# Performance work log

Measured on AMD Instinct MI355X. Metric: run time of the kernel, lower is better.

The kernel has to match this reference:

```python
import jax, jax.numpy as jnp
import numpy as np

N = 50000          # nodes
E = 500000         # edges (before self-loops)
G = 64             # graphs in batch
SC = 96            # scalar features
D = 32             # embedding dim
IN_DIM = SC + 5 * D  # 256
C = 128            # hidden_channels
H1 = 4             # heads in conv1
NUM_CLASSES = 5
V_OP, V_SRC, V_SINK, V_STR, V_PAY = 256, 512, 512, 128, 1024


def setup_inputs() -> dict:
    key = jax.random.key(0)
    ks = jax.random.split(key, 32)
    inp = {}
    inp['x_scalar'] = jax.random.normal(ks[0], (N, SC), jnp.float32)
    inp['x_opcode'] = jax.random.randint(ks[1], (N, 16), 0, V_OP)
    inp['x_source'] = jax.random.randint(ks[2], (N, 8), 0, V_SRC)
    inp['x_sink'] = jax.random.randint(ks[3], (N, 8), 0, V_SINK)
    inp['x_string_manip'] = jax.random.randint(ks[4], (N, 8), 0, V_STR)
    inp['x_payload'] = jax.random.randint(ks[5], (N, 8), 0, V_PAY)
    inp['edge_index'] = jax.random.randint(ks[6], (2, E), 0, N)
    # sorted graph ids with every graph non-empty
    inp['batch'] = (jnp.arange(N) * G) // N
    # learned params
    s = 0.05
    inp['emb_opcode'] = jax.random.normal(ks[7], (V_OP, D), jnp.float32)
    inp['emb_source'] = jax.random.normal(ks[8], (V_SRC, D), jnp.float32)
    inp['emb_sink'] = jax.random.normal(ks[9], (V_SINK, D), jnp.float32)
    inp['emb_string'] = jax.random.normal(ks[10], (V_STR, D), jnp.float32)
    inp['emb_payload'] = jax.random.normal(ks[11], (V_PAY, D), jnp.float32)
    inp['ln_g'] = jnp.ones((IN_DIM,), jnp.float32)
    inp['ln_b'] = jnp.zeros((IN_DIM,), jnp.float32)
    inp['W1'] = jax.random.normal(ks[12], (IN_DIM, H1 * C), jnp.float32) * s
    inp['att_src1'] = jax.random.normal(ks[13], (H1, C), jnp.float32) * s
    inp['att_dst1'] = jax.random.normal(ks[14], (H1, C), jnp.float32) * s
    inp['b1'] = jnp.zeros((H1 * C,), jnp.float32)
    inp['W2'] = jax.random.normal(ks[15], (H1 * C, C), jnp.float32) * s
    inp['att_src2'] = jax.random.normal(ks[16], (1, C), jnp.float32) * s
    inp['att_dst2'] = jax.random.normal(ks[17], (1, C), jnp.float32) * s
    inp['b2'] = jnp.zeros((C,), jnp.float32)
    inp['Wc1'] = jax.random.normal(ks[18], (C, C // 2), jnp.float32) * s
    inp['bc1'] = jnp.zeros((C // 2,), jnp.float32)
    inp['Wc2'] = jax.random.normal(ks[19], (C // 2, NUM_CLASSES), jnp.float32) * s
    inp['bc2'] = jnp.zeros((NUM_CLASSES,), jnp.float32)
    return inp


def _emb_feat(table, idx):
    # masked mean over the list dim; index 0 is padding
    e = table[idx]                                  # [N, L, D]
    mask = (idx != 0)[..., None].astype(e.dtype)    # [N, L, 1]
    return (e * mask).sum(1) / (mask.sum(1) + 1e-9)


def _layernorm(x, g, b, eps=1e-5):
    mu = x.mean(-1, keepdims=True)
    var = ((x - mu) ** 2).mean(-1, keepdims=True)
    return (x - mu) * jax.lax.rsqrt(var + eps) * g + b


def _gat_conv(x, W, att_src, att_dst, bias, src, dst, heads, out_ch, concat):
    n = x.shape[0]
    h = (x @ W).reshape(n, heads, out_ch)              # [N,H,C]
    a_src = (h * att_src).sum(-1)                      # [N,H]
    a_dst = (h * att_dst).sum(-1)                      # [N,H]
    e = jax.nn.leaky_relu(a_src[src] + a_dst[dst], 0.2)  # [E,H]
    m = jax.ops.segment_max(e, dst, num_segments=n)
    e = jnp.exp(e - m[dst])
    denom = jax.ops.segment_sum(e, dst, num_segments=n)
    alpha = e / (denom[dst] + 1e-16)                   # segment softmax over in-edges
    msg = h[src] * alpha[:, :, None]                   # [E,H,C]
    out = jax.ops.segment_sum(msg, dst, num_segments=n)  # [N,H,C]
    out = out.reshape(n, heads * out_ch) if concat else out.mean(1)
    return out + bias


def reference(x_scalar, x_opcode, x_source, x_sink, x_string_manip, x_payload,
              edge_index, batch,
              emb_opcode, emb_source, emb_sink, emb_string, emb_payload,
              ln_g, ln_b, W1, att_src1, att_dst1, b1,
              W2, att_src2, att_dst2, b2, Wc1, bc1, Wc2, bc2):
    n = x_scalar.shape[0]
    feats = jnp.concatenate([
        x_scalar,
        _emb_feat(emb_opcode, x_opcode),
        _emb_feat(emb_source, x_source),
        _emb_feat(emb_sink, x_sink),
        _emb_feat(emb_string, x_string_manip),
        _emb_feat(emb_payload, x_payload),
    ], axis=1)
    feats = _layernorm(feats, ln_g, ln_b)
    # add self loops (PyG GATConv default)
    loop = jnp.arange(n)
    src = jnp.concatenate([edge_index[0], loop])
    dst = jnp.concatenate([edge_index[1], loop])
    x = jax.nn.elu(_gat_conv(feats, W1, att_src1, att_dst1, b1, src, dst, H1, C, True))
    x = jax.nn.elu(_gat_conv(x, W2, att_src2, att_dst2, b2, src, dst, 1, C, True))
    # global max pool per graph (dropout layers are identity at inference)
    xp = jax.ops.segment_max(x, batch, num_segments=G)  # [G,C]
    hcls = jax.nn.relu(xp @ Wc1 + bc1)
    return hcls @ Wc2 + bc2
```

## Files before the change

### kernel.cpp

```cpp
#include <hip/hip_runtime.h>
#include <hip/hip_bf16.h>
#include <float.h>


#define LEAKY(e) ((e) > 0.f ? (e) : 0.2f * (e))
#define POOL_CH 32

typedef _Float16 half8 __attribute__((ext_vector_type(8)));
typedef float floatx4 __attribute__((ext_vector_type(4)));

__device__ __forceinline__ void async_copy16(const _Float16* gsrc,
                                             const _Float16* ldst) {
  __builtin_amdgcn_global_load_lds(
      (const __attribute__((address_space(1))) unsigned int*)gsrc,
      (__attribute__((address_space(3))) unsigned int*)ldst, 16, 0, 0);
}

__global__ __launch_bounds__(256) void feats_kernel(
    const float* __restrict__ xs, const int* __restrict__ xo,
    const int* __restrict__ xsrc, const int* __restrict__ xsk,
    const int* __restrict__ xst, const int* __restrict__ xp,
    const float* __restrict__ eo, const float* __restrict__ es,
    const float* __restrict__ ek, const float* __restrict__ et,
    const float* __restrict__ ep, const float* __restrict__ lng,
    const float* __restrict__ lnb, _Float16* __restrict__ feats, int n) {
  int node = blockIdx.x * 4 + (threadIdx.x >> 6);
  if (node >= n) return;
  int l = threadIdx.x & 63;

  int myidx = 0;
  if (l < 16)      myidx = xo[node * 16 + l];
  else if (l < 24) myidx = xsrc[node * 8 + (l - 16)];
  else if (l < 32) myidx = xsk[node * 8 + (l - 24)];
  else if (l < 40) myidx = xst[node * 8 + (l - 32)];
  else if (l < 48) myidx = xp[node * 8 + (l - 40)];

  const float* xrow = xs + (size_t)node * 96;
  float v0 = xrow[l];
  float v1, v2, v3;

  bool hi = (l >= 32);
  int d = l & 31;

  {
    float s = 0.f, c = 0.f;
#pragma unroll
    for (int j = 0; j < 16; j++) {
      int id = __shfl(myidx, j);
      if (hi && id != 0) { s += eo[(size_t)id * 32 + d]; c += 1.f; }
    }
    float sc = hi ? 0.f : xrow[64 + l];
    v1 = hi ? (s / (c + 1e-9f)) : sc;
  }
  {
    const float* tab = hi ? ek : es;
    int base = hi ? 24 : 16;
    float s = 0.f, c = 0.f;
#pragma unroll
    for (int j = 0; j < 8; j++) {
      int id = __shfl(myidx, base + j);
      if (id != 0) { s += tab[(size_t)id * 32 + d]; c += 1.f; }
    }
    v2 = s / (c + 1e-9f);
  }
  {
    const float* tab = hi ? ep : et;
    int base = hi ? 40 : 32;
    float s = 0.f, c = 0.f;
#pragma unroll
    for (int j = 0; j < 8; j++) {
      int id = __shfl(myidx, base + j);
      if (id != 0) { s += tab[(size_t)id * 32 + d]; c += 1.f; }
    }
    v3 = s / (c + 1e-9f);
  }

  float sum = v0 + v1 + v2 + v3;
  for (int o = 32; o; o >>= 1) sum += __shfl_xor(sum, o);
  float mu = sum * (1.f / 256.f);

  float d0 = v0 - mu, d1 = v1 - mu, d2 = v2 - mu, d3 = v3 - mu;
  float q = d0 * d0 + d1 * d1 + d2 * d2 + d3 * d3;
  for (int o = 32; o; o >>= 1) q += __shfl_xor(q, o);
  float rstd = rsqrtf(q * (1.f / 256.f) + 1e-5f);

  _Float16* frow = feats + (size_t)node * 256;
  frow[l]       = (_Float16)(d0 * rstd * lng[l] + lnb[l]);
  frow[64 + l]  = (_Float16)(d1 * rstd * lng[64 + l] + lnb[64 + l]);
  frow[128 + l] = (_Float16)(d2 * rstd * lng[128 + l] + lnb[128 + l]);
  frow[192 + l] = (_Float16)(d3 * rstd * lng[192 + l] + lnb[192 + l]);
}

__global__ __launch_bounds__(256) void transpose_both_f16(
    const float* __restrict__ W1, _Float16* __restrict__ Wt1,
    const float* __restrict__ W2, _Float16* __restrict__ Wt2) {
  int t = blockIdx.x * 256 + threadIdx.x;
  if (t < 256 * 512) {
    int n = t / 256, k = t - n * 256;
    Wt1[t] = (_Float16)W1[(size_t)k * 512 + n];
  } else {
    int u = t - 256 * 512;
    int n = u / 512, k = u - n * 512;
    Wt2[u] = (_Float16)W2[(size_t)k * 128 + n];
  }
}

__global__ __launch_bounds__(256) void gemm_f16_att(
    const _Float16* __restrict__ A, const _Float16* __restrict__ Bt,
    _Float16* __restrict__ C, const float* __restrict__ att_src,
    const float* __restrict__ att_dst, float* __restrict__ a_src_out,
    float* __restrict__ a_dst_out, int astride, int K, int N) {
  __shared__ __attribute__((aligned(16))) _Float16 As[128 * 32];
  __shared__ __attribute__((aligned(16))) _Float16 Bs[128 * 32];
  int m0 = blockIdx.y * 128;
  int n0 = blockIdx.x * 128;
  int tid = threadIdx.x;
  int wave = tid >> 6, lane = tid & 63;
  int wm = (wave >> 1) * 64, wn = (wave & 1) * 64;
  int lr = lane & 15, lq = lane >> 4;
  int wbase = tid & ~63;

  floatx4 acc[4][4] = {};

  for (int k0 = 0; k0 < K; k0 += 32) {
#pragma unroll
    for (int c = 0; c < 2; c++) {
      int sid = c * 256 + tid;
      int row = sid >> 2;
      int cs = (sid & 3) ^ (row & 3);
      const _Float16* ga = A + (size_t)(m0 + row) * K + k0 + cs * 8;
      const _Float16* gb = Bt + (size_t)(n0 + row) * K + k0 + cs * 8;
      async_copy16(ga, As + (size_t)(c * 256 + wbase) * 8);
      async_copy16(gb, Bs + (size_t)(c * 256 + wbase) * 8);
    }
    __syncthreads();

    half8 af[4], bf[4];
#pragma unroll
    for (int i = 0; i < 4; i++) {
      int row = wm + i * 16 + lr;
      af[i] = *(const half8*)(As + ((row << 2) + (lq ^ (row & 3))) * 8);
    }
#pragma unroll
    for (int j = 0; j < 4; j++) {
      int row = wn + j * 16 + lr;
      bf[j] = *(const half8*)(Bs + ((row << 2) + (lq ^ (row & 3))) * 8);
    }
#pragma unroll
    for (int i = 0; i < 4; i++)
#pragma unroll
      for (int j = 0; j < 4; j++)
        acc[i][j] =
            __builtin_amdgcn_mfma_f32_16x16x32_f16(af[i], bf[j], acc[i][j], 0, 0, 0);
    __syncthreads();
  }

#pragma unroll
  for (int i = 0; i < 4; i++) {
    int rbase = m0 + wm + i * 16 + lq * 4;
#pragma unroll
    for (int r = 0; r < 4; r++) {
      int row = rbase + r;
#pragma unroll
      for (int j = 0; j < 4; j++) {
        int col = n0 + wn + j * 16 + lr;
        C[(size_t)row * N + col] = (_Float16)acc[i][j][r];
      }
    }
  }

  float asv[4], adv[4];
#pragma unroll
  for (int j = 0; j < 4; j++) {
    int col = n0 + wn + j * 16 + lr;
    asv[j] = att_src[col];
    adv[j] = att_dst[col];
  }
  float ps[4][4], pd[4][4];
#pragma unroll
  for (int i = 0; i < 4; i++)
#pragma unroll
    for (int r = 0; r < 4; r++) {
      float s = 0.f, d = 0.f;
#pragma unroll
      for (int j = 0; j < 4; j++) {
        s += acc[i][j][r] * asv[j];
        d += acc[i][j][r] * adv[j];
      }
#pragma unroll
      for (int o = 1; o < 16; o <<= 1) {
        s += __shfl_xor(s, o);
        d += __shfl_xor(d, o);
      }
      ps[i][r] = s;
      pd[i][r] = d;
    }
  float* sred = (float*)&As[0];
  if (wn == 64 && lr == 0) {
#pragma unroll
    for (int i = 0; i < 4; i++)
#pragma unroll
      for (int r = 0; r < 4; r++) {
        int rl = wm + i * 16 + lq * 4 + r;
        sred[rl * 2] = ps[i][r];
        sred[rl * 2 + 1] = pd[i][r];
      }
  }
  __syncthreads();
  if (wn == 0 && lr == 0) {
    int hsel = n0 >> 7;
#pragma unroll
    for (int i = 0; i < 4; i++)
#pragma unroll
      for (int r = 0; r < 4; r++) {
        int rl = wm + i * 16 + lq * 4 + r;
        int row = m0 + rl;
        a_src_out[(size_t)row * astride + hsel] = ps[i][r] + sred[rl * 2];
        a_dst_out[(size_t)row * astride + hsel] = pd[i][r] + sred[rl * 2 + 1];
      }
  }
}

__global__ __launch_bounds__(256) void hist_kernel(const int* __restrict__ dst,
                                                   int* __restrict__ deg, int E) {
  int t = blockIdx.x * 256 + threadIdx.x;
  if (t < E) atomicAdd(&deg[dst[t]], 1);
}

__global__ __launch_bounds__(256) void scan_a(const int* __restrict__ deg,
                                              int* __restrict__ rowptr,
                                              int* __restrict__ bsum, int n) {
  __shared__ int sh[256];
  int b = blockIdx.x, t = threadIdx.x;
  int i = b * 256 + t;
  int v = (i < n) ? deg[i] + 1 : 0;
  sh[t] = v;
  __syncthreads();
  int x = v;
  for (int o = 1; o < 256; o <<= 1) {
    int y = (t >= o) ? sh[t - o] : 0;
    __syncthreads();
    x += y;
    sh[t] = x;
    __syncthreads();
  }
  if (i < n) rowptr[i] = x - v;
  if (t == 255) bsum[b] = x;
}

__global__ __launch_bounds__(256) void scan_b(int* __restrict__ bsum, int nb) {
  __shared__ int sh[256];
  int t = threadIdx.x;
  int v = (t < nb) ? bsum[t] : 0;
  sh[t] = v;
  __syncthreads();
  int x = v;
  for (int o = 1; o < 256; o <<= 1) {
    int y = (t >= o) ? sh[t - o] : 0;
    __syncthreads();
    x += y;
    sh[t] = x;
    __syncthreads();
  }
  if (t < nb) bsum[t] = x - v;
}

__global__ __launch_bounds__(256) void scan_c(int* __restrict__ rowptr,
                                              const int* __restrict__ bsum,
                                              int n, int total) {
  int i = blockIdx.x * 256 + threadIdx.x;
  if (i < n) rowptr[i] += bsum[blockIdx.x];
  else if (i == n) rowptr[n] = total;
}

__global__ __launch_bounds__(256) void fill_kernel(
    const int* __restrict__ src, const int* __restrict__ dst,
    const int* __restrict__ rowptr, int* __restrict__ cnt,
    int* __restrict__ csr_src, int E, int n) {
  int t = blockIdx.x * 256 + threadIdx.x;
  if (t < E) {
    int d = dst[t];
    int pos = rowptr[d] + atomicAdd(&cnt[d], 1);
    csr_src[pos] = src[t];
  } else if (t < E + n) {
    int i = t - E;
    csr_src[rowptr[i + 1] - 1] = i;
  }
}

__global__ __launch_bounds__(256) void gat1_agg(
    const _Float16* __restrict__ h1, const float* __restrict__ asrc,
    const float* __restrict__ adst, const int* __restrict__ rowptr,
    const int* __restrict__ csr_src, const float* __restrict__ bias,
    _Float16* __restrict__ out, int n) {
  int node = blockIdx.x * 4 + (threadIdx.x >> 6);
  if (node >= n) return;
  int l = threadIdx.x & 63;
  int hh = l >> 4;
  int li = l & 15;
  int r0 = rowptr[node];
  int deg = rowptr[node + 1] - r0;
  int cb = l * 8;

  float acc[8] = {};

  if (deg <= 64) {
    float adm = adst[node * 4 + hh];
    int s_reg[4];
    float ww[4];
    float m = -1e30f;
#pragma unroll
    for (int c = 0; c < 4; c++) {
      int k = c * 16 + li;
      int s = (k < deg) ? csr_src[r0 + k] : -1;
      s_reg[c] = s;
      float e = -1e30f;
      if (s >= 0) {
        float t = asrc[(size_t)s * 4 + hh] + adm;
        e = LEAKY(t);
      }
      ww[c] = e;
      m = fmaxf(m, e);
    }
#pragma unroll
    for (int o = 1; o < 16; o <<= 1) m = fmaxf(m, __shfl_xor(m, o));
    float sum = 0.f;
#pragma unroll
    for (int c = 0; c < 4; c++) {
      float w = (s_reg[c] >= 0) ? __expf(ww[c] - m) : 0.f;
      ww[c] = w;
      sum += w;
    }
#pragma unroll
    for (int o = 1; o < 16; o <<= 1) sum += __shfl_xor(sum, o);
    float sinv = 1.f / (sum + 1e-16f);
#pragma unroll
    for (int c = 0; c < 4; c++) ww[c] *= sinv;

#pragma unroll
    for (int c = 0; c < 4; c++) {
      int base = c * 16;
      if (base >= deg) break;
      int lim = min(16, deg - base);
      int jl = 0;
      for (; jl + 4 <= lim; jl += 4) {
        int s0 = __shfl(s_reg[c], jl);
        int s1 = __shfl(s_reg[c], jl + 1);
        int s2 = __shfl(s_reg[c], jl + 2);
        int s3 = __shfl(s_reg[c], jl + 3);
        float w0 = __shfl(ww[c], hh * 16 + jl);
        float w1 = __shfl(ww[c], hh * 16 + jl + 1);
        float w2 = __shfl(ww[c], hh * 16 + jl + 2);
        float w3 = __shfl(ww[c], hh * 16 + jl + 3);
        const half8 hv0 = *(const half8*)(h1 + (size_t)s0 * 512 + cb);
        const half8 hv1 = *(const half8*)(h1 + (size_t)s1 * 512 + cb);
        const half8 hv2 = *(const half8*)(h1 + (size_t)s2 * 512 + cb);
        const half8 hv3 = *(const half8*)(h1 + (size_t)s3 * 512 + cb);
#pragma unroll
        for (int q = 0; q < 8; q++)
          acc[q] += w0 * (float)hv0[q] + w1 * (float)hv1[q] +
                    w2 * (float)hv2[q] + w3 * (float)hv3[q];
      }
      for (; jl < lim; jl++) {
        int s0 = __shfl(s_reg[c], jl);
        float w0 = __shfl(ww[c], hh * 16 + jl);
        const half8 hv0 = *(const half8*)(h1 + (size_t)s0 * 512 + cb);
#pragma unroll
        for (int q = 0; q < 8; q++) acc[q] += w0 * (float)hv0[q];
      }
    }
  } else {
    float4 ad4 = *(const float4*)(adst + node * 4);
    float adv[4] = {ad4.x, ad4.y, ad4.z, ad4.w};
    float m[4] = {-1e30f, -1e30f, -1e30f, -1e30f};
    for (int k = l; k < deg; k += 64) {
      int s = csr_src[r0 + k];
      float4 av = *(const float4*)(asrc + (size_t)s * 4);
      float e;
      e = LEAKY(av.x + adv[0]); m[0] = fmaxf(m[0], e);
      e = LEAKY(av.y + adv[1]); m[1] = fmaxf(m[1], e);
      e = LEAKY(av.z + adv[2]); m[2] = fmaxf(m[2], e);
      e = LEAKY(av.w + adv[3]); m[3] = fmaxf(m[3], e);
    }
    for (int o = 1; o < 64; o <<= 1) {
#pragma unroll
      for (int h = 0; h < 4; h++) m[h] = fmaxf(m[h], __shfl_xor(m[h], o));
    }
    float sum[4] = {0.f, 0.f, 0.f, 0.f};
    for (int k = l; k < deg; k += 64) {
      int s = csr_src[r0 + k];
      float4 av = *(const float4*)(asrc + (size_t)s * 4);
      float e;
      e = LEAKY(av.x + adv[0]); sum[0] += __expf(e - m[0]);
      e = LEAKY(av.y + adv[1]); sum[1] += __expf(e - m[1]);
      e = LEAKY(av.z + adv[2]); sum[2] += __expf(e - m[2]);
      e = LEAKY(av.w + adv[3]); sum[3] += __expf(e - m[3]);
    }
    for (int o = 1; o < 64; o <<= 1) {
#pragma unroll
      for (int h = 0; h < 4; h++) sum[h] += __shfl_xor(sum[h], o);
    }
    float mm = m[hh];
    float sinv = 1.f / (sum[hh] + 1e-16f);
    float adm = adv[hh];
    for (int k = 0; k < deg; k++) {
      int s = csr_src[r0 + k];
      float a = asrc[(size_t)s * 4 + hh];
      float e = LEAKY(a + adm);
      float w = __expf(e - mm) * sinv;
      const half8 hv = *(const half8*)(h1 + (size_t)s * 512 + cb);
#pragma unroll
      for (int q = 0; q < 8; q++) acc[q] += w * (float)hv[q];
    }
  }

  const float* bp = bias + cb;
  half8 ov;
#pragma unroll
  for (int j = 0; j < 8; j++) {
    float r = acc[j] + bp[j];
    ov[j] = (_Float16)(r > 0.f ? r : (__expf(r) - 1.f));
  }
  *(half8*)(out + (size_t)node * 512 + cb) = ov;
}

__global__ __launch_bounds__(256) void gat2_agg(
    const _Float16* __restrict__ h2, const float* __restrict__ asrc,
    const float* __restrict__ adst, const int* __restrict__ rowptr,
    const int* __restrict__ csr_src, const float* __restrict__ bias,
    float* __restrict__ out, int n) {
  int node = blockIdx.x * 4 + (threadIdx.x >> 6);
  if (node >= n) return;
  int l = threadIdx.x & 63;
  int r0 = rowptr[node];
  int deg = rowptr[node + 1] - r0;
  int cb = l * 2;
  float a0 = 0.f, a1 = 0.f;

  if (deg <= 64) {
    float ad = adst[node];
    int s = (l < deg) ? csr_src[r0 + l] : -1;
    float e = -1e30f;
    if (s >= 0) {
      float t = asrc[s] + ad;
      e = LEAKY(t);
    }
    float m = e;
    for (int o = 1; o < 64; o <<= 1) m = fmaxf(m, __shfl_xor(m, o));
    float w = (s >= 0) ? __expf(e - m) : 0.f;
    float sum = w;
    for (int o = 1; o < 64; o <<= 1) sum += __shfl_xor(sum, o);
    w *= 1.f / (sum + 1e-16f);
    int j = 0;
    for (; j + 4 <= deg; j += 4) {
      int s0 = __shfl(s, j);
      int s1 = __shfl(s, j + 1);
      int s2 = __shfl(s, j + 2);
      int s3 = __shfl(s, j + 3);
      float w0 = __shfl(w, j);
      float w1 = __shfl(w, j + 1);
      float w2 = __shfl(w, j + 2);
      float w3 = __shfl(w, j + 3);
      const _Float16* hp0 = h2 + (size_t)s0 * 128 + cb;
      const _Float16* hp1 = h2 + (size_t)s1 * 128 + cb;
      const _Float16* hp2 = h2 + (size_t)s2 * 128 + cb;
      const _Float16* hp3 = h2 + (size_t)s3 * 128 + cb;
      float p00 = (float)hp0[0], p01 = (float)hp0[1];
      float p10 = (float)hp1[0], p11 = (float)hp1[1];
      float p20 = (float)hp2[0], p21 = (float)hp2[1];
      float p30 = (float)hp3[0], p31 = (float)hp3[1];
      a0 += w0 * p00 + w1 * p10 + w2 * p20 + w3 * p30;
      a1 += w0 * p01 + w1 * p11 + w2 * p21 + w3 * p31;
    }
    for (; j < deg; j++) {
      int sj = __shfl(s, j);
      float wj = __shfl(w, j);
      const _Float16* hp = h2 + (size_t)sj * 128 + cb;
      a0 += wj * (float)hp[0];
      a1 += wj * (float)hp[1];
    }
  } else {
    float ad = adst[node];
    float m = -1e30f;
    for (int k = l; k < deg; k += 64) {
      int s = csr_src[r0 + k];
      float e = LEAKY(asrc[s] + ad);
      m = fmaxf(m, e);
    }
    for (int o = 1; o < 64; o <<= 1) m = fmaxf(m, __shfl_xor(m, o));
    float sum = 0.f;
    for (int k = l; k < deg; k += 64) {
      int s = csr_src[r0 + k];
      float e = LEAKY(asrc[s] + ad);
      sum += __expf(e - m);
    }
    for (int o = 1; o < 64; o <<= 1) sum += __shfl_xor(sum, o);
    float sinv = 1.f / (sum + 1e-16f);
    for (int k = 0; k < deg; k++) {
      int s = csr_src[r0 + k];
      float e = LEAKY(asrc[s] + ad);
      float w = __expf(e - m) * sinv;
      const _Float16* hp = h2 + (size_t)s * 128 + cb;
      a0 += w * (float)hp[0];
      a1 += w * (float)hp[1];
    }
  }

  float ra = a0 + bias[cb];
  float rb = a1 + bias[cb + 1];
  out[(size_t)node * 128 + cb]     = ra > 0.f ? ra : (__expf(ra) - 1.f);
  out[(size_t)node * 128 + cb + 1] = rb > 0.f ? rb : (__expf(rb) - 1.f);
}

__device__ inline int lower_bound_i(const int* a, int n, int v) {
  int lo = 0, hi = n;
  while (lo < hi) {
    int mid = (lo + hi) >> 1;
    if (a[mid] < v) lo = mid + 1; else hi = mid;
  }
  return lo;
}

__global__ __launch_bounds__(128) void pool_partial(
    const float* __restrict__ x2, const int* __restrict__ batch,
    float* __restrict__ partial, int n) {
  int g = blockIdx.y;
  int j = blockIdx.x;
  int t = threadIdx.x;
  int start = lower_bound_i(batch, n, g);
  int end = lower_bound_i(batch, n, g + 1);
  int len = end - start;
  int c0 = start + (int)((long long)len * j / POOL_CH);
  int c1 = start + (int)((long long)len * (j + 1) / POOL_CH);
  float m = -FLT_MAX;
  for (int i = c0; i < c1; i++) m = fmaxf(m, x2[(size_t)i * 128 + t]);
  partial[((size_t)g * POOL_CH + j) * 128 + t] = m;
}

__global__ __launch_bounds__(128) void pool_final(
    const float* __restrict__ partial, float* __restrict__ pool) {
  int g = blockIdx.x;
  int t = threadIdx.x;
  float m = -FLT_MAX;
#pragma unroll
  for (int j = 0; j < POOL_CH; j++)
    m = fmaxf(m, partial[((size_t)g * POOL_CH + j) * 128 + t]);
  pool[g * 128 + t] = m;
}

__global__ __launch_bounds__(64) void classifier_kernel(
    const float* __restrict__ pool, const float* __restrict__ Wc1,
    const float* __restrict__ bc1, const float* __restrict__ Wc2,
    const float* __restrict__ bc2, float* __restrict__ out) {
  int g = blockIdx.x;
  int t = threadIdx.x;
  __shared__ float xp[128];
  __shared__ float hc[64];
  xp[t] = pool[g * 128 + t];
  xp[t + 64] = pool[g * 128 + 64 + t];
  __syncthreads();
  float s = bc1[t];
  for (int k = 0; k < 128; k++) s += xp[k] * Wc1[k * 64 + t];
  hc[t] = s > 0.f ? s : 0.f;
  __syncthreads();
  if (t < 5) {
    float o = bc2[t];
    for (int j = 0; j < 64; j++) o += hc[j] * Wc2[j * 5 + t];
    out[g * 5 + t] = o;
  }
}

extern "C" void kernel_launch(void* const* d_in, const int* in_sizes, int n_in,
                              void* d_out, int out_size, void* d_ws, size_t ws_size,
                              hipStream_t stream) {
  const float* x_scalar = (const float*)d_in[0];
  const int* x_opcode = (const int*)d_in[1];
  const int* x_source = (const int*)d_in[2];
  const int* x_sink = (const int*)d_in[3];
  const int* x_string = (const int*)d_in[4];
  const int* x_payload = (const int*)d_in[5];
  const int* edge_index = (const int*)d_in[6];
  const int* batch = (const int*)d_in[7];
  const float* emb_opcode = (const float*)d_in[8];
  const float* emb_source = (const float*)d_in[9];
  const float* emb_sink = (const float*)d_in[10];
  const float* emb_string = (const float*)d_in[11];
  const float* emb_payload = (const float*)d_in[12];
  const float* ln_g = (const float*)d_in[13];
  const float* ln_b = (const float*)d_in[14];
  const float* W1 = (const float*)d_in[15];
  const float* att_src1 = (const float*)d_in[16];
  const float* att_dst1 = (const float*)d_in[17];
  const float* b1 = (const float*)d_in[18];
  const float* W2 = (const float*)d_in[19];
  const float* att_src2 = (const float*)d_in[20];
  const float* att_dst2 = (const float*)d_in[21];
  const float* b2 = (const float*)d_in[22];
  const float* Wc1 = (const float*)d_in[23];
  const float* bc1 = (const float*)d_in[24];
  const float* Wc2 = (const float*)d_in[25];
  const float* bc2 = (const float*)d_in[26];
  float* out = (float*)d_out;

  const int N = in_sizes[0] / 96;
  const int E = in_sizes[6] / 2;
  const int G = out_size / 5;
  const int Npad = (N + 127) / 128 * 128;

  const int* e_src = edge_index;
  const int* e_dst = edge_index + E;

  char* w = (char*)d_ws;
  size_t o = 0;
  auto take = [&](size_t bytes) -> void* {
    void* p = w + o;
    o += (bytes + 255) & ~(size_t)255;
    return p;
  };
  char* regionA = (char*)take((size_t)Npad * 256 * 2);
  char* regionB = (char*)take((size_t)Npad * 512 * 2);
  _Float16* x1 = (_Float16*)take((size_t)Npad * 512 * 2);
  _Float16* Wt1 = (_Float16*)take((size_t)512 * 256 * 2);
  _Float16* Wt2 = (_Float16*)take((size_t)128 * 512 * 2);
  float* a_src1 = (float*)take((size_t)Npad * 4 * 4);
  float* a_dst1 = (float*)take((size_t)Npad * 4 * 4);
  float* a_src2 = (float*)take((size_t)Npad * 4);
  float* a_dst2 = (float*)take((size_t)Npad * 4);
  int* deg = (int*)take((size_t)N * 2 * 4);
  int* cnt = deg + N;
  int* rowptr = (int*)take((size_t)(N + 1) * 4);
  int* csr_src = (int*)take((size_t)(E + N) * 4);
  int* bsum = (int*)take(256 * 4);

  _Float16* feats = (_Float16*)regionA;
  _Float16* h2 = (_Float16*)regionA;
  float* partial = (float*)(regionA + (((size_t)Npad * 128 * 2 + 255) & ~(size_t)255));
  float* pool = partial + (size_t)G * POOL_CH * 128;
  _Float16* h1 = (_Float16*)regionB;
  float* x2 = (float*)regionB;

  hipMemsetAsync(deg, 0, (size_t)N * 2 * 4, stream);

  hist_kernel<<<(E + 255) / 256, 256, 0, stream>>>(e_dst, deg, E);
  int nb = (N + 255) / 256;
  scan_a<<<nb, 256, 0, stream>>>(deg, rowptr, bsum, N);
  scan_b<<<1, 256, 0, stream>>>(bsum, nb);
  scan_c<<<(N + 256) / 256, 256, 0, stream>>>(rowptr, bsum, N, E + N);
  fill_kernel<<<(E + N + 255) / 256, 256, 0, stream>>>(e_src, e_dst, rowptr, cnt,
                                                       csr_src, E, N);

  transpose_both_f16<<<(256 * 512 + 512 * 128 + 255) / 256, 256, 0, stream>>>(
      W1, Wt1, W2, Wt2);

  feats_kernel<<<(N + 3) / 4, 256, 0, stream>>>(
      x_scalar, x_opcode, x_source, x_sink, x_string, x_payload, emb_opcode,
      emb_source, emb_sink, emb_string, emb_payload, ln_g, ln_b, feats, N);

  int mblocks = Npad / 128;
  gemm_f16_att<<<dim3(512 / 128, mblocks), 256, 0, stream>>>(
      feats, Wt1, h1, att_src1, att_dst1, a_src1, a_dst1, 4, 256, 512);
  gat1_agg<<<(N + 3) / 4, 256, 0, stream>>>(h1, a_src1, a_dst1, rowptr, csr_src,
                                            b1, x1, N);

  gemm_f16_att<<<dim3(128 / 128, mblocks), 256, 0, stream>>>(
      x1, Wt2, h2, att_src2, att_dst2, a_src2, a_dst2, 1, 512, 128);
  gat2_agg<<<(N + 3) / 4, 256, 0, stream>>>(h2, a_src2, a_dst2, rowptr, csr_src,
                                            b2, x2, N);

  pool_partial<<<dim3(POOL_CH, G), 128, 0, stream>>>(x2, batch, partial, N);
  pool_final<<<G, 128, 0, stream>>>(partial, pool);
  classifier_kernel<<<G, 64, 0, stream>>>(pool, Wc1, bc1, Wc2, bc2, out);
}
```

Before: 441.8 us.

## Vectorize GAT2 gather with half8 loads, store x2 in fp16, drop scan_b

```diff
diff --git a/kernel.cpp b/kernel.cpp
--- a/kernel.cpp
+++ b/kernel.cpp
@@ -248,28 +248,14 @@
   if (t == 255) bsum[b] = x;
 }
 
-__global__ __launch_bounds__(256) void scan_b(int* __restrict__ bsum, int nb) {
-  __shared__ int sh[256];
-  int t = threadIdx.x;
-  int v = (t < nb) ? bsum[t] : 0;
-  sh[t] = v;
-  __syncthreads();
-  int x = v;
-  for (int o = 1; o < 256; o <<= 1) {
-    int y = (t >= o) ? sh[t - o] : 0;
-    __syncthreads();
-    x += y;
-    sh[t] = x;
-    __syncthreads();
-  }
-  if (t < nb) bsum[t] = x - v;
-}
-
 __global__ __launch_bounds__(256) void scan_c(int* __restrict__ rowptr,
                                               const int* __restrict__ bsum,
                                               int n, int total) {
-  int i = blockIdx.x * 256 + threadIdx.x;
-  if (i < n) rowptr[i] += bsum[blockIdx.x];
+  int b = blockIdx.x;
+  int off = 0;
+  for (int j = 0; j < b; j++) off += bsum[j];
+  int i = b * 256 + threadIdx.x;
+  if (i < n) rowptr[i] += off;
   else if (i == n) rowptr[n] = total;
 }
 
@@ -428,14 +414,12 @@
     const _Float16* __restrict__ h2, const float* __restrict__ asrc,
     const float* __restrict__ adst, const int* __restrict__ rowptr,
     const int* __restrict__ csr_src, const float* __restrict__ bias,
-    float* __restrict__ out, int n) {
+    _Float16* __restrict__ out, int n) {
   int node = blockIdx.x * 4 + (threadIdx.x >> 6);
   if (node >= n) return;
   int l = threadIdx.x & 63;
   int r0 = rowptr[node];
   int deg = rowptr[node + 1] - r0;
-  int cb = l * 2;
-  float a0 = 0.f, a1 = 0.f;
 
   if (deg <= 64) {
     float ad = adst[node];
@@ -451,33 +435,33 @@
     float sum = w;
     for (int o = 1; o < 64; o <<= 1) sum += __shfl_xor(sum, o);
     w *= 1.f / (sum + 1e-16f);
-    int j = 0;
-    for (; j + 4 <= deg; j += 4) {
-      int s0 = __shfl(s, j);
-      int s1 = __shfl(s, j + 1);
-      int s2 = __shfl(s, j + 2);
-      int s3 = __shfl(s, j + 3);
-      float w0 = __shfl(w, j);
-      float w1 = __shfl(w, j + 1);
-      float w2 = __shfl(w, j + 2);
-      float w3 = __shfl(w, j + 3);
-      const _Float16* hp0 = h2 + (size_t)s0 * 128 + cb;
-      const _Float16* hp1 = h2 + (size_t)s1 * 128 + cb;
-      const _Float16* hp2 = h2 + (size_t)s2 * 128 + cb;
-      const _Float16* hp3 = h2 + (size_t)s3 * 128 + cb;
-      float p00 = (float)hp0[0], p01 = (float)hp0[1];
-      float p10 = (float)hp1[0], p11 = (float)hp1[1];
-      float p20 = (float)hp2[0], p21 = (float)hp2[1];
-      float p30 = (float)hp3[0], p31 = (float)hp3[1];
-      a0 += w0 * p00 + w1 * p10 + w2 * p20 + w3 * p30;
-      a1 += w0 * p01 + w1 * p11 + w2 * p21 + w3 * p31;
-    }
-    for (; j < deg; j++) {
-      int sj = __shfl(s, j);
-      float wj = __shfl(w, j);
-      const _Float16* hp = h2 + (size_t)sj * 128 + cb;
-      a0 += wj * (float)hp[0];
-      a1 += wj * (float)hp[1];
+
+    int g4 = l >> 4;
+    int ch = (l & 15) * 8;
+    float acc[8] = {};
+    for (int j = 0; j < deg; j += 4) {
+      int je = j + g4;
+      int jc = min(je, 63);
+      int sj = __shfl(s, jc);
+      float wj = (je < deg) ? __shfl(w, jc) : 0.f;
+      if (sj < 0) sj = 0;
+      const half8 hv = *(const half8*)(h2 + (size_t)sj * 128 + ch);
+#pragma unroll
+      for (int q = 0; q < 8; q++) acc[q] += wj * (float)hv[q];
+    }
+#pragma unroll
+    for (int q = 0; q < 8; q++) {
+      acc[q] += __shfl_xor(acc[q], 16);
+      acc[q] += __shfl_xor(acc[q], 32);
+    }
+    if (l < 16) {
+      half8 ov;
+#pragma unroll
+      for (int q = 0; q < 8; q++) {
+        float r = acc[q] + bias[ch + q];
+        ov[q] = (_Float16)(r > 0.f ? r : (__expf(r) - 1.f));
+      }
+      *(half8*)(out + (size_t)node * 128 + ch) = ov;
     }
   } else {
     float ad = adst[node];
@@ -496,6 +480,8 @@
     }
     for (int o = 1; o < 64; o <<= 1) sum += __shfl_xor(sum, o);
     float sinv = 1.f / (sum + 1e-16f);
+    int cb = l * 2;
+    float a0 = 0.f, a1 = 0.f;
     for (int k = 0; k < deg; k++) {
       int s = csr_src[r0 + k];
       float e = LEAKY(asrc[s] + ad);
@@ -504,12 +490,11 @@
       a0 += w * (float)hp[0];
       a1 += w * (float)hp[1];
     }
-  }
-
-  float ra = a0 + bias[cb];
-  float rb = a1 + bias[cb + 1];
-  out[(size_t)node * 128 + cb]     = ra > 0.f ? ra : (__expf(ra) - 1.f);
-  out[(size_t)node * 128 + cb + 1] = rb > 0.f ? rb : (__expf(rb) - 1.f);
+    float ra = a0 + bias[cb];
+    float rb = a1 + bias[cb + 1];
+    out[(size_t)node * 128 + cb]     = (_Float16)(ra > 0.f ? ra : (__expf(ra) - 1.f));
+    out[(size_t)node * 128 + cb + 1] = (_Float16)(rb > 0.f ? rb : (__expf(rb) - 1.f));
+  }
 }
 
 __device__ inline int lower_bound_i(const int* a, int n, int v) {
@@ -522,7 +507,7 @@
 }
 
 __global__ __launch_bounds__(128) void pool_partial(
-    const float* __restrict__ x2, const int* __restrict__ batch,
+    const _Float16* __restrict__ x2, const int* __restrict__ batch,
     float* __restrict__ partial, int n) {
   int g = blockIdx.y;
   int j = blockIdx.x;
@@ -533,7 +518,7 @@
   int c0 = start + (int)((long long)len * j / POOL_CH);
   int c1 = start + (int)((long long)len * (j + 1) / POOL_CH);
   float m = -FLT_MAX;
-  for (int i = c0; i < c1; i++) m = fmaxf(m, x2[(size_t)i * 128 + t]);
+  for (int i = c0; i < c1; i++) m = fmaxf(m, (float)x2[(size_t)i * 128 + t]);
   partial[((size_t)g * POOL_CH + j) * 128 + t] = m;
 }
 
@@ -637,14 +622,13 @@
   float* partial = (float*)(regionA + (((size_t)Npad * 128 * 2 + 255) & ~(size_t)255));
   float* pool = partial + (size_t)G * POOL_CH * 128;
   _Float16* h1 = (_Float16*)regionB;
-  float* x2 = (float*)regionB;
+  _Float16* x2 = (_Float16*)regionB;
 
   hipMemsetAsync(deg, 0, (size_t)N * 2 * 4, stream);
 
   hist_kernel<<<(E + 255) / 256, 256, 0, stream>>>(e_dst, deg, E);
   int nb = (N + 255) / 256;
   scan_a<<<nb, 256, 0, stream>>>(deg, rowptr, bsum, N);
-  scan_b<<<1, 256, 0, stream>>>(bsum, nb);
   scan_c<<<(N + 256) / 256, 256, 0, stream>>>(rowptr, bsum, N, E + N);
   fill_kernel<<<(E + N + 255) / 256, 256, 0, stream>>>(e_src, e_dst, rowptr, cnt,
                                                        csr_src, E, N);
```

After: 440.4 us. Within noise of the previous version (-0.3%).
